# Performance work log

Measured on AMD Instinct MI355X. Metric: run time of the kernel, lower is better.

## Reference

```python
import jax, jax.numpy as jnp
import numpy as np

D_MODEL = 1024
NUM_HEADS = 16
HEAD_DIM = D_MODEL // NUM_HEADS


def setup_inputs() -> dict:
    key = jax.random.key(0)
    k1, k2, k3, k4, k5 = jax.random.split(key, 5)
    x = jax.random.normal(k1, (2, 2048, D_MODEL), dtype=jnp.float32)
    # PyTorch Linear-style params: weight [out, in], bias [out]
    s = 1.0 / np.sqrt(D_MODEL)
    w_qkv = jax.random.uniform(k2, (3 * D_MODEL, D_MODEL), jnp.float32, -s, s)
    b_qkv = jax.random.uniform(k3, (3 * D_MODEL,), jnp.float32, -s, s)
    w_out = jax.random.uniform(k4, (D_MODEL, D_MODEL), jnp.float32, -s, s)
    b_out = jax.random.uniform(k5, (D_MODEL,), jnp.float32, -s, s)
    return {"x": x, "w_qkv": w_qkv, "b_qkv": b_qkv, "w_out": w_out, "b_out": b_out}


def reference(x, w_qkv, b_qkv, w_out, b_out):
    B, S, D = x.shape
    H, hd = NUM_HEADS, HEAD_DIM
    # fused QKV projection: (B,S,3D)
    qkv = jnp.einsum('bsd,ed->bse', x, w_qkv) + b_qkv
    # reshape to (B,S,H,3*hd) then permute to (B,H,S,3*hd) then chunk
    qkv = qkv.reshape(B, S, H, 3 * hd).transpose(0, 2, 1, 3)
    q, k, v = jnp.split(qkv, 3, axis=-1)  # each (B,H,S,hd)
    scores = jnp.einsum('bhqd,bhkd->bhqk', q, k) / np.sqrt(hd).astype(jnp.float32)
    attn = jax.nn.softmax(scores, axis=-1)  # dropout is identity in eval
    out = jnp.einsum('bhqk,bhkd->bhqd', attn, v)
    out = out.transpose(0, 2, 1, 3).reshape(B, S, D)
    return jnp.einsum('bsd,ed->bse', out, w_out) + b_out
```

## Files before the change

kernel.cpp:

```cpp
#include <hip/hip_runtime.h>
#include <hip/hip_bf16.h>

#define D_MODEL 1024
#define S_LEN   2048
#define NBATCH  2
#define NHEADS  16
#define HDIM    64
#define DQKV    3072

typedef short bf16x8 __attribute__((ext_vector_type(8)));
typedef float f32x4  __attribute__((ext_vector_type(4)));
typedef float f32x16 __attribute__((ext_vector_type(16)));
typedef unsigned int u32;

__device__ __forceinline__ unsigned short bf16_rne(float f) {
    unsigned u = __float_as_uint(f);
    return (unsigned short)((u + 0x7FFFu + ((u >> 16) & 1u)) >> 16);
}

__global__ __launch_bounds__(256) void cast_f32_bf16(
    const float* __restrict__ in, unsigned short* __restrict__ out, int n4)
{
    int i = blockIdx.x * blockDim.x + threadIdx.x;
    const int stride = gridDim.x * blockDim.x;
    for (; i < n4; i += stride) {
        float4 v = ((const float4*)in)[i];
        ((ushort4*)out)[i] = make_ushort4(bf16_rne(v.x), bf16_rne(v.y),
                                          bf16_rne(v.z), bf16_rne(v.w));
    }
}

__device__ __forceinline__ void gld_lds16(const unsigned short* g, unsigned short* l) {
    __builtin_amdgcn_global_load_lds(
        (const __attribute__((address_space(1))) unsigned int*)g,
        (__attribute__((address_space(3))) unsigned int*)l, 16, 0, 0);
}

__device__ __forceinline__ bf16x8 lds_frag(const unsigned short* base, int row, int e8) {
    int byte = (row << 7) + (e8 << 4);
    byte ^= (row & 7) << 4;
    return *(const bf16x8*)((const char*)base + byte);
}

#define GEMM_CORE(A_, B_, K_)                                                  \
    __shared__ unsigned short sA[128 * 32];                                    \
    __shared__ unsigned short sB[128 * 32];                                    \
    const int tid  = threadIdx.x;                                              \
    const int lane = tid & 63;                                                 \
    const int wid  = tid >> 6;                                                 \
    const int bm = blockIdx.y * 128, bn = blockIdx.x * 128;                    \
    const int wr = (wid >> 1) * 64, wc = (wid & 1) * 64;                       \
    const int half = wid & 1;                                                  \
    const unsigned short* gsrc = (wid < 2) ? A_ : B_;                          \
    unsigned short* ldst = ((wid < 2) ? sA : sB) + half * 2048;                \
    const int brow = ((wid < 2) ? bm : bn) + half * 64;                        \
    const size_t rowbase = (size_t)(brow + (lane >> 2)) * K_ + (lane & 3) * 8; \
    f32x4 acc[4][4];                                                           \
    _Pragma("unroll")                                                          \
    for (int m = 0; m < 4; ++m)                                                \
        _Pragma("unroll")                                                      \
        for (int n = 0; n < 4; ++n)                                            \
            acc[m][n] = f32x4{0.f, 0.f, 0.f, 0.f};                             \
    const int frA = (wr + (lane & 15)) * 32 + (lane >> 4) * 8;                 \
    const int frB = (wc + (lane & 15)) * 32 + (lane >> 4) * 8;                 \
    for (int k0 = 0; k0 < K_; k0 += 32) {                                      \
        __syncthreads();                                                       \
        const unsigned short* g = gsrc + rowbase + k0;                         \
        _Pragma("unroll")                                                      \
        for (int c = 0; c < 4; ++c)                                            \
            gld_lds16(g + (size_t)c * 16 * K_, ldst + c * 512);                \
        __syncthreads();                                                       \
        bf16x8 a[4], b[4];                                                     \
        _Pragma("unroll")                                                      \
        for (int m = 0; m < 4; ++m) a[m] = *(const bf16x8*)&sA[frA + m * 512]; \
        _Pragma("unroll")                                                      \
        for (int n = 0; n < 4; ++n) b[n] = *(const bf16x8*)&sB[frB + n * 512]; \
        _Pragma("unroll")                                                      \
        for (int m = 0; m < 4; ++m)                                            \
            _Pragma("unroll")                                                  \
            for (int n = 0; n < 4; ++n)                                        \
                acc[m][n] = __builtin_amdgcn_mfma_f32_16x16x32_bf16(           \
                    a[m], b[n], acc[m][n], 0, 0, 0);                           \
    }

__global__ __launch_bounds__(256) void gemm_mfma_out(
    const unsigned short* __restrict__ A, const unsigned short* __restrict__ B,
    const float* __restrict__ bias, float* __restrict__ C, int M, int N, int K)
{
    GEMM_CORE(A, B, K)
    #pragma unroll
    for (int n = 0; n < 4; ++n) {
        const int col = bn + wc + n * 16 + (lane & 15);
        const float bv = bias[col];
        #pragma unroll
        for (int m = 0; m < 4; ++m) {
            const int row0 = bm + wr + m * 16 + (lane >> 4) * 4;
            #pragma unroll
            for (int j = 0; j < 4; ++j)
                C[(size_t)(row0 + j) * N + col] = acc[m][n][j] + bv;
        }
    }
}

__global__ __launch_bounds__(256) void gemm_mfma_qkv(
    const unsigned short* __restrict__ A, const unsigned short* __restrict__ B,
    const float* __restrict__ bias,
    unsigned short* __restrict__ Qs, unsigned short* __restrict__ Ks,
    unsigned short* __restrict__ Vt, int M, int N, int K)
{
    GEMM_CORE(A, B, K)
    #pragma unroll
    for (int n = 0; n < 4; ++n) {
        const int col = bn + wc + n * 16 + (lane & 15);
        const unsigned head = (unsigned)col / 192u;
        const int c = col - (int)head * 192;
        const int cls = c >> 6;
        const float bv = bias[col];
        #pragma unroll
        for (int m = 0; m < 4; ++m) {
            const int row0 = bm + wr + m * 16 + (lane >> 4) * 4;
            #pragma unroll
            for (int j = 0; j < 4; ++j) {
                const int row = row0 + j;
                const int bb = row >> 11, ss = row & 2047;
                float val = acc[m][n][j] + bv;
                if (cls == 0) val *= 0.18033688011110918f;
                const unsigned short v = bf16_rne(val);
                if (cls == 2) {
                    Vt[((size_t)(bb * NHEADS + head) * HDIM + (c - 128)) * S_LEN + ss] = v;
                } else {
                    const size_t idx = ((size_t)(bb * NHEADS + head) * S_LEN + ss) * HDIM + (c & 63);
                    if (cls == 0) Qs[idx] = v; else Ks[idx] = v;
                }
            }
        }
    }
}

__global__ __launch_bounds__(512) void attn_mfma_kernel(
    const unsigned short* __restrict__ Qs, const unsigned short* __restrict__ Ks,
    const unsigned short* __restrict__ Vt, unsigned short* __restrict__ ob)
{
    __shared__ unsigned short smem[2][2][2][4096];

    const int tid  = threadIdx.x;
    const int lane = tid & 63;
    const int wid  = tid >> 6;
    const int wq   = wid & 3;
    const int par  = wid >> 2;
    const int h    = lane >> 5;
    const int qcol = lane & 31;

    const int bid = blockIdx.x;
    const int lb  = (bid & 7) * 64 + (bid >> 3);
    const int qt  = lb & 15;
    const int bh  = lb >> 4;
    const int q0  = qt * 128 + wq * 32;

    bf16x8 qf[4];
    {
        const unsigned short* qr = Qs + ((size_t)bh * S_LEN + q0 + qcol) * HDIM + h * 8;
        #pragma unroll
        for (int ks = 0; ks < 4; ++ks) qf[ks] = *(const bf16x8*)(qr + ks * 16);
    }

    const unsigned short* gKV = (wq < 2) ? Ks : Vt;
    const int cls   = wq >> 1;
    const int cbase = (wq & 1) * 4;
    const int r8    = lane >> 3;
    const int colb  = ((lane & 7) ^ r8) << 3;

    float m_run = -1e30f, l_run = 0.0f;
    f32x16 accO[2];
    #pragma unroll
    for (int m = 0; m < 2; ++m)
        #pragma unroll
        for (int r = 0; r < 16; ++r) accO[m][r] = 0.0f;

    #define STAGE(buf, kt)                                                          \
        do {                                                                        \
            unsigned short* pl_ = &smem[buf][par][cls][0];                          \
            if (cls == 0) {                                                         \
                const unsigned short* g_ = gKV + ((size_t)bh * S_LEN + (kt) + r8) * HDIM + colb; \
                _Pragma("unroll")                                                   \
                for (int c_ = 0; c_ < 4; ++c_)                                      \
                    gld_lds16(g_ + (size_t)(cbase + c_) * 8 * HDIM,                 \
                              pl_ + (cbase + c_) * 512);                            \
            } else {                                                                \
                const unsigned short* g_ = gKV + ((size_t)bh * HDIM + r8) * S_LEN + (kt) + colb; \
                _Pragma("unroll")                                                   \
                for (int c_ = 0; c_ < 4; ++c_)                                      \
                    gld_lds16(g_ + (size_t)(cbase + c_) * 8 * S_LEN,                \
                              pl_ + (cbase + c_) * 512);                            \
            }                                                                       \
        } while (0)

    STAGE(0, par * 64);
    __syncthreads();

    int cur = 0;
    for (int it = 0; it < S_LEN / 128; ++it) {
        if (it + 1 < S_LEN / 128) STAGE(cur ^ 1, (it + 1) * 128 + par * 64);

        const unsigned short* cK = &smem[cur][par][0][0];
        const unsigned short* cV = &smem[cur][par][1][0];

        f32x16 accS[2];
        #pragma unroll
        for (int mm = 0; mm < 2; ++mm)
            #pragma unroll
            for (int r = 0; r < 16; ++r) accS[mm][r] = 0.0f;

        __builtin_amdgcn_s_setprio(1);
        #pragma unroll
        for (int ks = 0; ks < 4; ++ks) {
            const int e8 = ks * 2 + h;
            #pragma unroll
            for (int mm = 0; mm < 2; ++mm) {
                bf16x8 ak = lds_frag(cK, mm * 32 + qcol, e8);
                accS[mm] = __builtin_amdgcn_mfma_f32_32x32x16_bf16(ak, qf[ks], accS[mm], 0, 0, 0);
            }
        }
        __builtin_amdgcn_s_setprio(0);

        float p[32];
        #pragma unroll
        for (int mm = 0; mm < 2; ++mm)
            #pragma unroll
            for (int r = 0; r < 16; ++r) p[mm * 16 + r] = accS[mm][r];

        float t16[16];
        #pragma unroll
        for (int i = 0; i < 16; ++i) t16[i] = fmaxf(p[i], p[i + 16]);
        float t8[8];
        #pragma unroll
        for (int i = 0; i < 8; ++i) t8[i] = fmaxf(t16[i], t16[i + 8]);
        float t4[4];
        #pragma unroll
        for (int i = 0; i < 4; ++i) t4[i] = fmaxf(t8[i], t8[i + 4]);
        float mx = fmaxf(fmaxf(t4[0], t4[1]), fmaxf(t4[2], t4[3]));
        mx = fmaxf(mx, __shfl_xor(mx, 32));

        if (!__all(mx <= m_run + 8.0f)) {
            const float mnew = fmaxf(m_run, mx);
            const float corr = __builtin_amdgcn_exp2f(m_run - mnew);
            m_run = mnew;
            l_run *= corr;
            #pragma unroll
            for (int m = 0; m < 2; ++m)
                #pragma unroll
                for (int r = 0; r < 16; ++r) accO[m][r] *= corr;
        }

        #pragma unroll
        for (int i = 0; i < 32; ++i) p[i] = __builtin_amdgcn_exp2f(p[i] - m_run);
        float s16[16];
        #pragma unroll
        for (int i = 0; i < 16; ++i) s16[i] = p[i] + p[i + 16];
        float s8[8];
        #pragma unroll
        for (int i = 0; i < 8; ++i) s8[i] = s16[i] + s16[i + 8];
        float s4[4];
        #pragma unroll
        for (int i = 0; i < 4; ++i) s4[i] = s8[i] + s8[i + 4];
        float rs = (s4[0] + s4[1]) + (s4[2] + s4[3]);
        rs += __shfl_xor(rs, 32);
        l_run += rs;

        const bool hib = (h != 0);
        #pragma unroll
        for (int mm = 0; mm < 2; ++mm) {
            u32 wh_[8], sh_[8];
            #pragma unroll
            for (int i = 0; i < 8; ++i) {
                const float pe = p[mm * 16 + 2 * i], po = p[mm * 16 + 2 * i + 1];
                asm("v_cvt_pk_bf16_f32 %0, %1, %2" : "=v"(wh_[i]) : "v"(pe), "v"(po));
            }
            #pragma unroll
            for (int i = 0; i < 8; ++i) sh_[i] = __shfl_xor(wh_[i], 32);
            #pragma unroll
            for (int cc = 0; cc < 2; ++cc) {
                const int b0 = cc * 4;
                union { u32 w[4]; bf16x8 v; } uh;
                uh.w[0] = hib ? sh_[b0 + 2] : wh_[b0 + 0];
                uh.w[1] = hib ? sh_[b0 + 3] : wh_[b0 + 1];
                uh.w[2] = hib ? wh_[b0 + 2] : sh_[b0 + 0];
                uh.w[3] = hib ? wh_[b0 + 3] : sh_[b0 + 1];
                const int e8 = (mm * 2 + cc) * 2 + h;
                #pragma unroll
                for (int mdc = 0; mdc < 2; ++mdc) {
                    bf16x8 vf = lds_frag(cV, mdc * 32 + qcol, e8);
                    accO[mdc] = __builtin_amdgcn_mfma_f32_32x32x16_bf16(vf, uh.v, accO[mdc], 0, 0, 0);
                }
            }
        }

        __syncthreads();
        cur ^= 1;
    }
    #undef STAGE

    float* mbuf = (float*)&smem[0][0][0][0];
    if (par == 1) {
        float* dst = mbuf + ((size_t)(wq * 64 + lane)) * 35;
        #pragma unroll
        for (int mdc = 0; mdc < 2; ++mdc)
            #pragma unroll
            for (int r = 0; r < 16; ++r) dst[mdc * 16 + r] = accO[mdc][r];
        dst[32] = m_run;
        dst[33] = l_run;
    }
    __syncthreads();
    if (par == 0) {
        const float* src = mbuf + ((size_t)(wq * 64 + lane)) * 35;
        const float m2 = src[32], l2 = src[33];
        const float mt = fmaxf(m_run, m2);
        const float w1 = __builtin_amdgcn_exp2f(m_run - mt);
        const float w2 = __builtin_amdgcn_exp2f(m2 - mt);
        const float inv = 1.0f / (l_run * w1 + l2 * w2);

        const int bb = bh >> 4, hh = bh & 15;
        const int ss = q0 + qcol;
        unsigned short* po = ob + ((size_t)(bb * S_LEN + ss)) * D_MODEL + hh * HDIM;
        #pragma unroll
        for (int mdc = 0; mdc < 2; ++mdc)
            #pragma unroll
            for (int r = 0; r < 16; r += 2) {
                const int d = mdc * 32 + (r & 3) + 8 * (r >> 2) + 4 * h;
                const float v0 = (accO[mdc][r]     * w1 + src[mdc * 16 + r]     * w2) * inv;
                const float v1 = (accO[mdc][r + 1] * w1 + src[mdc * 16 + r + 1] * w2) * inv;
                *(u32*)(po + d) = ((u32)bf16_rne(v1) << 16) | bf16_rne(v0);
            }
    }
}

extern "C" void kernel_launch(void* const* d_in, const int* in_sizes, int n_in,
                              void* d_out, int out_size, void* d_ws, size_t ws_size,
                              hipStream_t stream)
{
    const float* x     = (const float*)d_in[0];
    const float* w_qkv = (const float*)d_in[1];
    const float* b_qkv = (const float*)d_in[2];
    const float* w_out = (const float*)d_in[3];
    const float* b_out = (const float*)d_in[4];
    float* out = (float*)d_out;

    const int M = NBATCH * S_LEN;
    const size_t PL = (size_t)32 * S_LEN * HDIM;

    unsigned short* xb  = (unsigned short*)d_ws;
    unsigned short* wqb = xb  + PL;
    unsigned short* wob = wqb + (size_t)DQKV * D_MODEL;
    unsigned short* Qs  = wob + (size_t)D_MODEL * D_MODEL;
    unsigned short* Ks  = Qs  + PL;
    unsigned short* Vt  = Ks  + PL;
    unsigned short* aob = Vt  + PL;

    dim3 blk(256);
    cast_f32_bf16<<<1024, blk, 0, stream>>>(x, xb, (int)(PL / 4));
    cast_f32_bf16<<<1024, blk, 0, stream>>>(w_qkv, wqb, DQKV * D_MODEL / 4);
    cast_f32_bf16<<<512,  blk, 0, stream>>>(w_out, wob, D_MODEL * D_MODEL / 4);

    gemm_mfma_qkv<<<dim3(DQKV / 128, M / 128), blk, 0, stream>>>(
        xb, wqb, b_qkv, Qs, Ks, Vt, M, DQKV, D_MODEL);

    attn_mfma_kernel<<<dim3(512), dim3(512), 0, stream>>>(Qs, Ks, Vt, aob);

    gemm_mfma_out<<<dim3(D_MODEL / 128, M / 128), blk, 0, stream>>>(
        aob, wob, b_out, out, M, D_MODEL, D_MODEL);
}
```

Measured before the change: 145.2 us.

## Double GEMM K-tile with swizzled LDS and compute softmax row sums via MFMA

The GEMM core now stages 64-wide K tiles, twice as many per barrier pair, using an XOR-swizzled LDS layout read through lds_frag. This halves the number of sync points and should cut LDS bank conflicts. In attention, the per-row softmax sum is no longer a VALU reduction tree with a cross-lane shuffle. It is accumulated by an extra MFMA against a ones vector, which moves ALU work onto the matrix unit. The cost is 16 more accumulator registers, one extra MFMA per PV step, and summing bf16-rounded probabilities instead of fp32 ones.

Result: no change. 146.2 us (+0.7%).

```diff
diff --git a/kernel.cpp b/kernel.cpp
--- a/kernel.cpp
+++ b/kernel.cpp
@@ -43,8 +43,8 @@
 }
 
 #define GEMM_CORE(A_, B_, K_)                                                  \
-    __shared__ unsigned short sA[128 * 32];                                    \
-    __shared__ unsigned short sB[128 * 32];                                    \
+    __shared__ unsigned short sA[128 * 64];                                    \
+    __shared__ unsigned short sB[128 * 64];                                    \
     const int tid  = threadIdx.x;                                              \
     const int lane = tid & 63;                                                 \
     const int wid  = tid >> 6;                                                 \
@@ -52,35 +52,41 @@
     const int wr = (wid >> 1) * 64, wc = (wid & 1) * 64;                       \
     const int half = wid & 1;                                                  \
     const unsigned short* gsrc = (wid < 2) ? A_ : B_;                          \
-    unsigned short* ldst = ((wid < 2) ? sA : sB) + half * 2048;                \
+    unsigned short* ldst = ((wid < 2) ? sA : sB) + half * 4096;                \
     const int brow = ((wid < 2) ? bm : bn) + half * 64;                        \
-    const size_t rowbase = (size_t)(brow + (lane >> 2)) * K_ + (lane & 3) * 8; \
+    const int r8_  = lane >> 3;                                                \
+    const int colb_ = ((lane & 7) ^ r8_) << 3;                                 \
+    const size_t rowbase = (size_t)(brow + r8_) * K_ + colb_;                  \
     f32x4 acc[4][4];                                                           \
     _Pragma("unroll")                                                          \
     for (int m = 0; m < 4; ++m)                                                \
         _Pragma("unroll")                                                      \
         for (int n = 0; n < 4; ++n)                                            \
             acc[m][n] = f32x4{0.f, 0.f, 0.f, 0.f};                             \
-    const int frA = (wr + (lane & 15)) * 32 + (lane >> 4) * 8;                 \
-    const int frB = (wc + (lane & 15)) * 32 + (lane >> 4) * 8;                 \
-    for (int k0 = 0; k0 < K_; k0 += 32) {                                      \
+    for (int k0 = 0; k0 < K_; k0 += 64) {                                      \
         __syncthreads();                                                       \
         const unsigned short* g = gsrc + rowbase + k0;                         \
         _Pragma("unroll")                                                      \
-        for (int c = 0; c < 4; ++c)                                            \
-            gld_lds16(g + (size_t)c * 16 * K_, ldst + c * 512);                \
+        for (int c = 0; c < 8; ++c)                                            \
+            gld_lds16(g + (size_t)c * 8 * K_, ldst + c * 512);                 \
         __syncthreads();                                                       \
-        bf16x8 a[4], b[4];                                                     \
         _Pragma("unroll")                                                      \
-        for (int m = 0; m < 4; ++m) a[m] = *(const bf16x8*)&sA[frA + m * 512]; \
-        _Pragma("unroll")                                                      \
-        for (int n = 0; n < 4; ++n) b[n] = *(const bf16x8*)&sB[frB + n * 512]; \
-        _Pragma("unroll")                                                      \
-        for (int m = 0; m < 4; ++m)                                            \
+        for (int ks2 = 0; ks2 < 2; ++ks2) {                                    \
+            const int e8 = (lane >> 4) + ks2 * 4;                              \
+            bf16x8 a[4], b[4];                                                 \
+            _Pragma("unroll")                                                  \
+            for (int m = 0; m < 4; ++m)                                        \
+                a[m] = lds_frag(sA, wr + m * 16 + (lane & 15), e8);            \
             _Pragma("unroll")                                                  \
             for (int n = 0; n < 4; ++n)                                        \
-                acc[m][n] = __builtin_amdgcn_mfma_f32_16x16x32_bf16(           \
-                    a[m], b[n], acc[m][n], 0, 0, 0);                           \
+                b[n] = lds_frag(sB, wc + n * 16 + (lane & 15), e8);            \
+            _Pragma("unroll")                                                  \
+            for (int m = 0; m < 4; ++m)                                        \
+                _Pragma("unroll")                                              \
+                for (int n = 0; n < 4; ++n)                                    \
+                    acc[m][n] = __builtin_amdgcn_mfma_f32_16x16x32_bf16(       \
+                        a[m], b[n], acc[m][n], 0, 0, 0);                       \
+        }                                                                      \
     }
 
 __global__ __launch_bounds__(256) void gemm_mfma_out(
@@ -164,18 +170,21 @@
         for (int ks = 0; ks < 4; ++ks) qf[ks] = *(const bf16x8*)(qr + ks * 16);
     }
 
+    bf16x8 onesv;
+    #pragma unroll
+    for (int i = 0; i < 8; ++i) onesv[i] = (short)0x3F80;
+
     const unsigned short* gKV = (wq < 2) ? Ks : Vt;
     const int cls   = wq >> 1;
     const int cbase = (wq & 1) * 4;
     const int r8    = lane >> 3;
     const int colb  = ((lane & 7) ^ r8) << 3;
 
-    float m_run = -1e30f, l_run = 0.0f;
+    float m_run = -1e30f;
     f32x16 accO[2];
+    f32x16 accL;
     #pragma unroll
-    for (int m = 0; m < 2; ++m)
-        #pragma unroll
-        for (int r = 0; r < 16; ++r) accO[m][r] = 0.0f;
+    for (int r = 0; r < 16; ++r) { accO[0][r] = 0.0f; accO[1][r] = 0.0f; accL[r] = 0.0f; }
 
     #define STAGE(buf, kt)                                                          \
         do {                                                                        \
@@ -207,9 +216,7 @@
 
         f32x16 accS[2];
         #pragma unroll
-        for (int mm = 0; mm < 2; ++mm)
-            #pragma unroll
-            for (int r = 0; r < 16; ++r) accS[mm][r] = 0.0f;
+        for (int r = 0; r < 16; ++r) { accS[0][r] = 0.0f; accS[1][r] = 0.0f; }
 
         __builtin_amdgcn_s_setprio(1);
         #pragma unroll
@@ -223,15 +230,9 @@
         }
         __builtin_amdgcn_s_setprio(0);
 
-        float p[32];
-        #pragma unroll
-        for (int mm = 0; mm < 2; ++mm)
-            #pragma unroll
-            for (int r = 0; r < 16; ++r) p[mm * 16 + r] = accS[mm][r];
-
         float t16[16];
         #pragma unroll
-        for (int i = 0; i < 16; ++i) t16[i] = fmaxf(p[i], p[i + 16]);
+        for (int i = 0; i < 16; ++i) t16[i] = fmaxf(accS[0][i], accS[1][i]);
         float t8[8];
         #pragma unroll
         for (int i = 0; i < 8; ++i) t8[i] = fmaxf(t16[i], t16[i + 8]);
@@ -245,27 +246,17 @@
             const float mnew = fmaxf(m_run, mx);
             const float corr = __builtin_amdgcn_exp2f(m_run - mnew);
             m_run = mnew;
-            l_run *= corr;
-            #pragma unroll
-            for (int m = 0; m < 2; ++m)
-                #pragma unroll
-                for (int r = 0; r < 16; ++r) accO[m][r] *= corr;
-        }
-
-        #pragma unroll
-        for (int i = 0; i < 32; ++i) p[i] = __builtin_amdgcn_exp2f(p[i] - m_run);
-        float s16[16];
-        #pragma unroll
-        for (int i = 0; i < 16; ++i) s16[i] = p[i] + p[i + 16];
-        float s8[8];
-        #pragma unroll
-        for (int i = 0; i < 8; ++i) s8[i] = s16[i] + s16[i + 8];
-        float s4[4];
-        #pragma unroll
-        for (int i = 0; i < 4; ++i) s4[i] = s8[i] + s8[i + 4];
-        float rs = (s4[0] + s4[1]) + (s4[2] + s4[3]);
-        rs += __shfl_xor(rs, 32);
-        l_run += rs;
+            #pragma unroll
+            for (int r = 0; r < 16; ++r) {
+                accO[0][r] *= corr; accO[1][r] *= corr; accL[r] *= corr;
+            }
+        }
+
+        #pragma unroll
+        for (int mm = 0; mm < 2; ++mm)
+            #pragma unroll
+            for (int r = 0; r < 16; ++r)
+                accS[mm][r] = __builtin_amdgcn_exp2f(accS[mm][r] - m_run);
 
         const bool hib = (h != 0);
         #pragma unroll
@@ -273,7 +264,7 @@
             u32 wh_[8], sh_[8];
             #pragma unroll
             for (int i = 0; i < 8; ++i) {
-                const float pe = p[mm * 16 + 2 * i], po = p[mm * 16 + 2 * i + 1];
+                const float pe = accS[mm][2 * i], po = accS[mm][2 * i + 1];
                 asm("v_cvt_pk_bf16_f32 %0, %1, %2" : "=v"(wh_[i]) : "v"(pe), "v"(po));
             }
             #pragma unroll
@@ -287,11 +278,11 @@
                 uh.w[2] = hib ? wh_[b0 + 2] : sh_[b0 + 0];
                 uh.w[3] = hib ? wh_[b0 + 3] : sh_[b0 + 1];
                 const int e8 = (mm * 2 + cc) * 2 + h;
-                #pragma unroll
-                for (int mdc = 0; mdc < 2; ++mdc) {
-                    bf16x8 vf = lds_frag(cV, mdc * 32 + qcol, e8);
-                    accO[mdc] = __builtin_amdgcn_mfma_f32_32x32x16_bf16(vf, uh.v, accO[mdc], 0, 0, 0);
-                }
+                bf16x8 vf0 = lds_frag(cV, qcol, e8);
+                bf16x8 vf1 = lds_frag(cV, 32 + qcol, e8);
+                accO[0] = __builtin_amdgcn_mfma_f32_32x32x16_bf16(vf0, uh.v, accO[0], 0, 0, 0);
+                accO[1] = __builtin_amdgcn_mfma_f32_32x32x16_bf16(vf1, uh.v, accO[1], 0, 0, 0);
+                accL    = __builtin_amdgcn_mfma_f32_32x32x16_bf16(onesv, uh.v, accL, 0, 0, 0);
             }
         }
 
@@ -299,6 +290,8 @@
         cur ^= 1;
     }
     #undef STAGE
+
+    const float l_run = accL[0];
 
     float* mbuf = (float*)&smem[0][0][0][0];
     if (par == 1) {
```
